# Optimization experiments

Hardware: AMD Instinct MI355X
Metric: run time of the kernel (lower is better)

Reference implementation:

```python
import jax, jax.numpy as jnp
import numpy as np
import math

Q_SHAPES = [(20, 30), (10, 15), (5, 8)]
S_SHAPES = [(20, 30), (10, 15), (5, 8)]
C_IN = 256
C_OUT = 256
NUM_HEADS = 8


def _rel_indices(q_shapes, s_shapes):
    # Faithful translation of QSGA.get_rel_indices: block matrix over pyramid levels.
    rows = []
    for hq, wq in q_shapes:
        cols = []
        for hs, ws in s_shapes:
            ind = np.arange(ws)[None, :] / ws - np.arange(hq)[:, None] / hq  # [hq, ws]
            sc = math.sqrt(ws * hq)
            indx = np.tile(ind, (wq, hs)) * sc                              # [hq*wq, hs*ws]
            indy = np.repeat(np.repeat(ind, wq, axis=0), hs, axis=1) * sc   # [hq*wq, hs*ws]
            indd = indx ** 2 + indy ** 2
            cols.append(np.stack([indd, indx, indy], axis=-1))
        rows.append(np.concatenate(cols, axis=1))
    return jnp.asarray(np.concatenate(rows, axis=0)[None].astype(np.float32))  # [1, Nq, Ns, 3]


def setup_inputs() -> dict:
    key = jax.random.key(0)
    ks = jax.random.split(key, 8)
    B, M = 2, 5
    Nq = sum(h * w for h, w in Q_SHAPES)
    Ns = sum(h * w for h, w in S_SHAPES)
    std = 0.02
    # local_init: v = identity, pos_proj weight zero except col0 = -alphas, gating = ones
    min_a, max_a = 0.002, 0.2
    alphas = np.array([min_a + (max_a - min_a) / NUM_HEADS ** 2.5 * i ** 2.5 for i in range(NUM_HEADS)], np.float32)
    Wp = np.zeros((NUM_HEADS, 3), np.float32)
    Wp[:, 0] = -alphas
    return {
        "q_feat": jax.random.normal(ks[0], (B, Nq, C_IN), jnp.float32),
        "s_feat": jax.random.normal(ks[1], (M, Ns, C_IN), jnp.float32),
        "rel_indices": _rel_indices(Q_SHAPES, S_SHAPES),
        "Wq": jax.random.normal(ks[2], (C_OUT, C_IN), jnp.float32) * std,
        "bq": jnp.zeros((C_OUT,), jnp.float32),
        "Wk": jax.random.normal(ks[3], (C_OUT, C_IN), jnp.float32) * std,
        "bk": jnp.zeros((C_OUT,), jnp.float32),
        "Wv": jnp.eye(C_OUT, C_IN, dtype=jnp.float32),
        "bv": jnp.zeros((C_OUT,), jnp.float32),
        "Wp": jnp.asarray(Wp),
        "bp": jnp.zeros((NUM_HEADS,), jnp.float32),
        "Wo": jax.random.normal(ks[4], (C_OUT, C_OUT), jnp.float32) * std,
        "bo": jnp.zeros((C_OUT,), jnp.float32),
        "gating": jnp.ones((NUM_HEADS,), jnp.float32),
    }


def reference(q_feat, s_feat, rel_indices, Wq, bq, Wk, bk, Wv, bv, Wp, bp, Wo, bo, gating):
    B, Nq, _ = q_feat.shape
    M, Ns, _ = s_feat.shape
    H = gating.shape[0]
    C = Wq.shape[0]
    Dh = C // H
    scale = Dh ** -0.5
    # projections -> [B,H,Nq,Dh], [M,H,Ns,Dh]
    q = (q_feat @ Wq.T + bq).reshape(B, Nq, H, Dh).transpose(0, 2, 1, 3)
    k = (s_feat @ Wk.T + bk).reshape(M, Ns, H, Dh).transpose(0, 2, 1, 3)
    # content scores over all (query image, support image) pairs: [B,M,H,Nq,Ns]
    patch = jnp.einsum('bhqd,mhsd->bmhqs', q, k) * scale
    patch = jax.nn.softmax(patch, axis=-1)
    # positional scores: [1,Nq,Ns,3] -> [1,H,Nq,Ns]
    pos = jax.nn.softmax((rel_indices @ Wp.T + bp).transpose(0, 3, 1, 2), axis=-1)
    g = jax.nn.sigmoid(gating)[None, None, :, None, None]  # [1,1,H,1,1]
    attn = (1.0 - g) * patch + g * pos[:, None]            # broadcast pos over B,M
    attn = attn / attn.sum(axis=-1, keepdims=True)
    v = (s_feat @ Wv.T + bv).reshape(M, Ns, H, Dh).transpose(0, 2, 1, 3)  # [M,H,Ns,Dh]
    out = jnp.einsum('bmhqs,mhsd->bmhqd', attn, v)          # [B,M,H,Nq,Dh]
    out = out.transpose(0, 1, 3, 2, 4).reshape(B, M, Nq, C)  # [B,M,Nq,C]
    return out @ Wo.T + bo
```

## Files before the change

kernel.cpp:

```cpp
#include <hip/hip_runtime.h>
#include <hip/hip_bf16.h>
#include <math.h>

#define B_ 2
#define M_ 5
#define H_ 8
#define C_ 256
#define DH 32
#define NQ 790
#define NS 790
#define QT32 25
#define VROW 800
#define PPAD 800

typedef __attribute__((ext_vector_type(8))) __bf16 bf16x8;
typedef __attribute__((ext_vector_type(16))) float f32x16;
typedef unsigned int u32;
typedef unsigned short u16;

#define LOG2E 1.4426950408889634f

static __device__ __forceinline__ u16 bf16bits(float v) {
  union { __bf16 h; u16 u; } x; x.h = (__bf16)v; return x.u;
}
static __device__ __forceinline__ u32 pack2bf(float a, float b) {
  union { __bf16 h[2]; u32 u; } x; x.h[0] = (__bf16)a; x.h[1] = (__bf16)b; return x.u;
}

#define POS_N 395
#define GEMM0 395
#define PADBLK 544

#define PROJ_STEP(ACC, BY)                                                 \
  {                                                                        \
    int bcol_ = (BY) * 64 + wc * 32 + lo;                                  \
    const float* wf_ = Wm + (size_t)bcol_ * C_ + k0;                       \
    float4 g0_ = *(const float4*)wf_, g1_ = *(const float4*)(wf_ + 4);     \
    bf16x8 b_;                                                             \
    b_[0]=(__bf16)g0_.x; b_[1]=(__bf16)g0_.y; b_[2]=(__bf16)g0_.z; b_[3]=(__bf16)g0_.w; \
    b_[4]=(__bf16)g1_.x; b_[5]=(__bf16)g1_.y; b_[6]=(__bf16)g1_.z; b_[7]=(__bf16)g1_.w; \
    ACC = __builtin_amdgcn_mfma_f32_32x32x16_bf16(a_, b_, ACC, 0, 0, 0);   \
  }

#define STORE_QK(ACC, BY)                                                  \
  {                                                                        \
    int bcol_ = (BY) * 64 + wc * 32 + lo;                                  \
    float bvv_ = bias[bcol_];                                              \
    _Pragma("unroll")                                                      \
    for (int r_ = 0; r_ < 16; ++r_) {                                      \
      int row_ = (r_ & 3) + 8 * (r_ >> 2) + 4 * hi;                        \
      int grow_ = grow0 + wr * 32 + row_;                                  \
      if (grow_ < R) {                                                     \
        float v_ = (ACC[r_] + bvv_) * scale;                               \
        int seg_ = grow_ / 790, srow_ = grow_ - seg_ * 790;                \
        size_t addr_ = ((size_t)(seg_ * H_ + (bcol_ >> 5)) * 790 + srow_) * 32 + (bcol_ & 31); \
        outp[addr_] = bf16bits(v_);                                        \
      }                                                                    \
    }                                                                      \
  }

#define STORE_V(ACC, BY)                                                   \
  {                                                                        \
    int bcol_ = (BY) * 64 + wc * 32 + lo;                                  \
    float bvv_ = bias[bcol_];                                              \
    int cIn_ = wc * 32 + lo;                                               \
    _Pragma("unroll")                                                      \
    for (int r_ = 0; r_ < 16; ++r_) {                                      \
      int row_ = (r_ & 3) + 8 * (r_ >> 2) + 4 * hi;                        \
      Tls[cIn_][wr * 32 + row_] = bf16bits(ACC[r_] + bvv_);                \
    }                                                                      \
    __syncthreads();                                                       \
    {                                                                      \
      int c_l = tid >> 2, g_l = (tid & 3) * 16;                            \
      int gcol = (BY) * 64 + c_l;                                          \
      int g0v = grow0 + g_l;                                               \
      u16 vals_[16];                                                       \
      _Pragma("unroll")                                                    \
      for (int i_ = 0; i_ < 16; ++i_) vals_[i_] = Tls[c_l][g_l + i_];      \
      int mA_ = g0v / 790, mB_ = (g0v + 15) / 790;                         \
      u16* dst_ = vT2 + (size_t)gcol * (M_ * VROW);                        \
      if (mB_ < M_ && mA_ == mB_) {                                        \
        size_t base_ = (size_t)mA_ * VROW + (g0v - mA_ * 790);             \
        *(uint4*)(dst_ + base_)     = *(uint4*)(vals_);                    \
        *(uint4*)(dst_ + base_ + 8) = *(uint4*)(vals_ + 8);                \
      } else {                                                             \
        _Pragma("unroll")                                                  \
        for (int i_ = 0; i_ < 16; ++i_) {                                  \
          int g_ = g0v + i_;                                               \
          if (g_ < M_ * 790) {                                             \
            int mm_ = g_ / 790, ss_ = g_ - mm_ * 790;                      \
            dst_[(size_t)mm_ * VROW + ss_] = vals_[i_];                    \
          }                                                                \
        }                                                                  \
      }                                                                    \
    }                                                                      \
    __syncthreads();                                                       \
  }

__global__ __launch_bounds__(256) void stage1(const float* __restrict__ qf,
    const float* __restrict__ sf, const float* __restrict__ rel,
    const float* __restrict__ Wq, const float* __restrict__ bq,
    const float* __restrict__ Wk, const float* __restrict__ bk,
    const float* __restrict__ Wv, const float* __restrict__ bv,
    const float* __restrict__ Wp, const float* __restrict__ bp,
    u16* __restrict__ qb, u16* __restrict__ kb, u16* __restrict__ vT2,
    u16* __restrict__ pp, float qscale) {
  __shared__ u16 Tls[64][72];
  int bid = blockIdx.x;
  int tid = threadIdx.x;

  if (bid < POS_N) {
    int wave = tid >> 6, lane = tid & 63;
    int q = bid * 2 + (wave >> 1);
    int h0 = (wave & 1) * 4;
    float rd[13], rx[13], ry[13];
#pragma unroll
    for (int t = 0; t < 13; ++t) {
      int s = lane + 64 * t;
      if (s < NS) {
        const float* rp = rel + ((size_t)q * NS + s) * 3;
        rd[t] = rp[0]; rx[t] = rp[1]; ry[t] = rp[2];
      } else { rd[t] = 0.f; rx[t] = 0.f; ry[t] = 0.f; }
    }
    for (int h = h0; h < h0 + 4; ++h) {
      float w0 = Wp[h * 3] * LOG2E, w1 = Wp[h * 3 + 1] * LOG2E,
            w2 = Wp[h * 3 + 2] * LOG2E, b = bp[h] * LOG2E;
      float lg[13], mx = -1e30f;
#pragma unroll
      for (int t = 0; t < 13; ++t) {
        int s = lane + 64 * t;
        float v = rd[t] * w0 + rx[t] * w1 + ry[t] * w2 + b;
        lg[t] = (s < NS) ? v : -1e30f;
        mx = fmaxf(mx, lg[t]);
      }
#pragma unroll
      for (int off = 32; off; off >>= 1) mx = fmaxf(mx, __shfl_xor(mx, off));
      float sm = 0.f;
#pragma unroll
      for (int t = 0; t < 13; ++t) { lg[t] = exp2f(lg[t] - mx); sm += lg[t]; }
#pragma unroll
      for (int off = 32; off; off >>= 1) sm += __shfl_xor(sm, off);
      float inv = 1.f / sm;
#pragma unroll
      for (int t = 0; t < 13; ++t) {
        int s = lane + 64 * t;
        if (s < PPAD)
          pp[((size_t)h * NQ + q) * PPAD + s] = (s < NS) ? bf16bits(lg[t] * inv) : (u16)0;
      }
    }
    return;
  }

  if (bid == PADBLK) {
    int c = tid;
#pragma unroll
    for (int m = 0; m < M_; ++m) {
      u32* p = (u32*)(vT2 + (size_t)c * (M_ * VROW) + m * VROW + 790);
#pragma unroll
      for (int i = 0; i < 5; ++i) p[i] = 0;
    }
    return;
  }

  int j = bid - GEMM0;
  const float* A; const float* Wm; const float* bias; int R; float scale; int role; int bx;
  if (j < 25)      { A = qf; Wm = Wq; bias = bq; R = B_ * NQ; scale = qscale; role = 0; bx = j; }
  else if (j < 87) { A = sf; Wm = Wk; bias = bk; R = M_ * NS; scale = 1.f;    role = 1; bx = j - 25; }
  else             { A = sf; Wm = Wv; bias = bv; R = M_ * NS; scale = 1.f;    role = 2; bx = j - 87; }

  int wave = tid >> 6, lane = tid & 63;
  int lo = lane & 31, hi = lane >> 5;
  int wr = wave >> 1, wc = wave & 1;
  int grow0 = bx * 64;
  int arow = grow0 + wr * 32 + lo;
  int ar = arow < R ? arow : R - 1;

  f32x16 acc0, acc1, acc2, acc3;
#pragma unroll
  for (int r = 0; r < 16; ++r) { acc0[r] = 0.f; acc1[r] = 0.f; acc2[r] = 0.f; acc3[r] = 0.f; }
#pragma unroll
  for (int kk = 0; kk < 16; ++kk) {
    int k0 = kk * 16 + hi * 8;
    const float* af = A + (size_t)ar * C_ + k0;
    float4 f0 = *(const float4*)af, f1 = *(const float4*)(af + 4);
    bf16x8 a_;
    a_[0]=(__bf16)f0.x; a_[1]=(__bf16)f0.y; a_[2]=(__bf16)f0.z; a_[3]=(__bf16)f0.w;
    a_[4]=(__bf16)f1.x; a_[5]=(__bf16)f1.y; a_[6]=(__bf16)f1.z; a_[7]=(__bf16)f1.w;
    PROJ_STEP(acc0, 0);
    PROJ_STEP(acc1, 1);
    PROJ_STEP(acc2, 2);
    PROJ_STEP(acc3, 3);
  }

  if (role < 2) {
    u16* outp = (role == 0) ? qb : kb;
    STORE_QK(acc0, 0);
    STORE_QK(acc1, 1);
    STORE_QK(acc2, 2);
    STORE_QK(acc3, 3);
  } else {
    STORE_V(acc0, 0);
    STORE_V(acc1, 1);
    STORE_V(acc2, 2);
    STORE_V(acc3, 3);
  }
}

static __device__ __forceinline__ void wave_range(int wave, int& st, int& en) {
  st = wave * 6 + (wave ? 1 : 0);
  en = st + (wave ? 6 : 7);
}

#define SM_PV(c_, OACC, ZR, FV0, FV1)                                      \
  {                                                                        \
    float p_[16];                                                          \
    _Pragma("unroll")                                                      \
    for (int r_ = 0; r_ < 16; ++r_) p_[r_] = exp2f(c_[r_]);                \
    float s0_ = p_[0]+p_[1],  s1_ = p_[2]+p_[3];                           \
    float s2_ = p_[4]+p_[5],  s3_ = p_[6]+p_[7];                           \
    float s4_ = p_[8]+p_[9],  s5_ = p_[10]+p_[11];                         \
    float s6_ = p_[12]+p_[13], s7_ = p_[14]+p_[15];                        \
    s0_ += s1_; s2_ += s3_; s4_ += s5_; s6_ += s7_;                        \
    s0_ += s2_; s4_ += s6_;                                                \
    float ts_ = s0_ + s4_;                                                 \
    { float xa_ = ts_, xb_ = ts_;                                          \
      asm("v_permlane32_swap_b32 %0, %1" : "+v"(xa_), "+v"(xb_));          \
      ZR += xa_ + xb_; }                                                   \
    u32 pk_[8];                                                            \
    _Pragma("unroll")                                                      \
    for (int t_ = 0; t_ < 8; ++t_) pk_[t_] = pack2bf(p_[2*t_], p_[2*t_+1]); \
    asm("v_permlane32_swap_b32 %0, %1" : "+v"(pk_[0]), "+v"(pk_[2]));      \
    asm("v_permlane32_swap_b32 %0, %1" : "+v"(pk_[1]), "+v"(pk_[3]));      \
    asm("v_permlane32_swap_b32 %0, %1" : "+v"(pk_[4]), "+v"(pk_[6]));      \
    asm("v_permlane32_swap_b32 %0, %1" : "+v"(pk_[5]), "+v"(pk_[7]));      \
    union { u32 u[4]; bf16x8 v; } pa_, pb_;                                \
    pa_.u[0] = pk_[0]; pa_.u[1] = pk_[1]; pa_.u[2] = pk_[2]; pa_.u[3] = pk_[3]; \
    pb_.u[0] = pk_[4]; pb_.u[1] = pk_[5]; pb_.u[2] = pk_[6]; pb_.u[3] = pk_[7]; \
    OACC = __builtin_amdgcn_mfma_f32_32x32x16_bf16(FV0, pa_.v, OACC, 0, 0, 0); \
    OACC = __builtin_amdgcn_mfma_f32_32x32x16_bf16(FV1, pb_.v, OACC, 0, 0, 0); \
  }

#define TILE_BODY(KC0,KC1,VC0,VC1,PC0,PC1, KN0,KN1,VN0,VN1,PN0,PN1, IT, NT) \
  {                                                                        \
    int srn_ = (NT) * 32 + lo; if (srn_ >= NS) srn_ = NS - 1;              \
    KN0 = *(const bf16x8*)(kbase + (size_t)srn_ * 32 + hi8);               \
    KN1 = *(const bf16x8*)(kbase + (size_t)srn_ * 32 + 16 + hi8);          \
    VN0 = *(const bf16x8*)(vbase + (NT) * 32 + hi8);                       \
    VN1 = *(const bf16x8*)(vbase + (NT) * 32 + 16 + hi8);                  \
    PN0 = *(const bf16x8*)(pbase + (NT) * 32 + hi8);                       \
    PN1 = *(const bf16x8*)(pbase + (NT) * 32 + 16 + hi8);                  \
    f32x16 c0_ = kZero, c1_ = kZero;                                       \
    c0_ = __builtin_amdgcn_mfma_f32_32x32x16_bf16(KC0, fq00, c0_, 0, 0, 0);\
    c0_ = __builtin_amdgcn_mfma_f32_32x32x16_bf16(KC1, fq01, c0_, 0, 0, 0);\
    c1_ = __builtin_amdgcn_mfma_f32_32x32x16_bf16(KC0, fq10, c1_, 0, 0, 0);\
    c1_ = __builtin_amdgcn_mfma_f32_32x32x16_bf16(KC1, fq11, c1_, 0, 0, 0);\
    Opos = __builtin_amdgcn_mfma_f32_32x32x16_bf16(VC0, PC0, Opos, 0, 0, 0);\
    Opos = __builtin_amdgcn_mfma_f32_32x32x16_bf16(VC1, PC1, Opos, 0, 0, 0);\
    if ((IT) == 24) {                                                      \
      _Pragma("unroll")                                                    \
      for (int r_ = 0; r_ < 16; ++r_) {                                    \
        int sl_ = (r_ & 3) + 8 * (r_ >> 2) + 4 * hi;                       \
        if (768 + sl_ >= NS) { c0_[r_] = -1e30f; c1_[r_] = -1e30f; }       \
      }                                                                    \
    }                                                                      \
    SM_PV(c0_, O0, Z0, VC0, VC1);                                          \
    SM_PV(c1_, O1, Z1, VC0, VC1);                                          \
  }

__global__ __launch_bounds__(256, 2) void attn2(const u16* __restrict__ qb,
    const u16* __restrict__ kb, const u16* __restrict__ vT2,
    const u16* __restrict__ pp, const float* __restrict__ gating,
    u16* __restrict__ opb) {
  int logical = (blockIdx.x & 7) * 125 + (blockIdx.x >> 3);
  int m  = logical % M_;
  int r2 = logical / M_;
  int qt = r2 % QT32;
  int h  = r2 / QT32;
  int tid = threadIdx.x;
  int wave = tid >> 6, lane = tid & 63;
  int lo = lane & 31, hi = lane >> 5, hi8 = hi * 8;
  int qg = qt * 32 + lo;
  int qc = qg < NQ ? qg : NQ - 1;

  const u16* qp0 = qb + ((size_t)(0 * H_ + h) * NQ + qc) * 32 + hi8;
  const u16* qp1 = qb + ((size_t)(1 * H_ + h) * NQ + qc) * 32 + hi8;
  bf16x8 fq00 = *(const bf16x8*)qp0;
  bf16x8 fq01 = *(const bf16x8*)(qp0 + 16);
  bf16x8 fq10 = *(const bf16x8*)qp1;
  bf16x8 fq11 = *(const bf16x8*)(qp1 + 16);
  const u16* kbase = kb + ((size_t)(m * H_ + h) * NS) * 32;
  const u16* vbase = vT2 + (size_t)(h * DH + lo) * (M_ * VROW) + m * VROW;
  const u16* pbase = pp + ((size_t)h * NQ + qc) * PPAD;

  f32x16 O0, O1, Opos, kZero;
#pragma unroll
  for (int r = 0; r < 16; ++r) { O0[r] = 0.f; O1[r] = 0.f; Opos[r] = 0.f; kZero[r] = 0.f; }
  float Z0 = 0.f, Z1 = 0.f;
  int st, en; wave_range(wave, st, en);

  bf16x8 ak0, ak1, av0, av1, ap0, ap1, bk0, bk1, bv0, bv1, bp0, bp1;
  {
    int sr0 = st * 32 + lo; if (sr0 >= NS) sr0 = NS - 1;
    ak0 = *(const bf16x8*)(kbase + (size_t)sr0 * 32 + hi8);
    ak1 = *(const bf16x8*)(kbase + (size_t)sr0 * 32 + 16 + hi8);
    av0 = *(const bf16x8*)(vbase + st * 32 + hi8);
    av1 = *(const bf16x8*)(vbase + st * 32 + 16 + hi8);
    ap0 = *(const bf16x8*)(pbase + st * 32 + hi8);
    ap1 = *(const bf16x8*)(pbase + st * 32 + 16 + hi8);
  }
  int it = st;
  while (it + 2 <= en) {
    TILE_BODY(ak0, ak1, av0, av1, ap0, ap1, bk0, bk1, bv0, bv1, bp0, bp1, it, it + 1);
    int nt2 = (it + 2 < en) ? it + 2 : it + 1;
    TILE_BODY(bk0, bk1, bv0, bv1, bp0, bp1, ak0, ak1, av0, av1, ap0, ap1, it + 1, nt2);
    it += 2;
  }
  if (it < en) TILE_BODY(ak0, ak1, av0, av1, ap0, ap1, bk0, bk1, bv0, bv1, bp0, bp1, it, it);

  __shared__ float Os[4][32][33];
  __shared__ float Zs[4][32];
  float g = 1.f / (1.f + __expf(-gating[h]));
  int d = tid & 31, qi = tid >> 5;
  float oc0[4], oc1[4];

#pragma unroll
  for (int r = 0; r < 16; ++r) {
    int dd = (r & 3) + 8 * (r >> 2) + 4 * hi;
    Os[wave][dd][lo] = O0[r];
  }
  if (hi == 0) Zs[wave][lo] = Z0;
  __syncthreads();
#pragma unroll
  for (int k = 0; k < 4; ++k) {
    int ql = qi + 8 * k;
    float zg = Zs[0][ql] + Zs[1][ql] + Zs[2][ql] + Zs[3][ql];
    float oc = Os[0][d][ql] + Os[1][d][ql] + Os[2][d][ql] + Os[3][d][ql];
    oc0[k] = (1.f - g) * oc / zg;
  }
  __syncthreads();

#pragma unroll
  for (int r = 0; r < 16; ++r) {
    int dd = (r & 3) + 8 * (r >> 2) + 4 * hi;
    Os[wave][dd][lo] = O1[r];
  }
  if (hi == 0) Zs[wave][lo] = Z1;
  __syncthreads();
#pragma unroll
  for (int k = 0; k < 4; ++k) {
    int ql = qi + 8 * k;
    float zg = Zs[0][ql] + Zs[1][ql] + Zs[2][ql] + Zs[3][ql];
    float oc = Os[0][d][ql] + Os[1][d][ql] + Os[2][d][ql] + Os[3][d][ql];
    oc1[k] = (1.f - g) * oc / zg;
  }
  __syncthreads();

#pragma unroll
  for (int r = 0; r < 16; ++r) {
    int dd = (r & 3) + 8 * (r >> 2) + 4 * hi;
    Os[wave][dd][lo] = Opos[r];
  }
  __syncthreads();
  u16* out0 = opb + ((size_t)(0 * M_ + m) * NQ) * C_ + h * DH + d;
  u16* out1 = opb + ((size_t)(1 * M_ + m) * NQ) * C_ + h * DH + d;
#pragma unroll
  for (int k = 0; k < 4; ++k) {
    int ql = qi + 8 * k;
    int qgl = qt * 32 + ql;
    if (qgl < NQ) {
      float op = Os[0][d][ql] + Os[1][d][ql] + Os[2][d][ql] + Os[3][d][ql];
      out0[(size_t)qgl * C_] = bf16bits(oc0[k] + g * op);
      out1[(size_t)qgl * C_] = bf16bits(oc1[k] + g * op);
    }
  }
}

__global__ __launch_bounds__(256) void out_gemm(const u16* __restrict__ Ap,
    const float* __restrict__ W, const float* __restrict__ bias,
    float* __restrict__ outp, int R) {
  int tid = threadIdx.x;
  int wave = tid >> 6, lane = tid & 63;
  int lo = lane & 31, hi = lane >> 5;
  int wr = wave >> 1, wc = wave & 1;
  int arow = blockIdx.x * 64 + wr * 32 + lo;
  int ar = arow < R ? arow : R - 1;
  int bcolA = blockIdx.y * 128 + wc * 32 + lo;
  int bcolB = bcolA + 64;
  f32x16 accA, accB;
#pragma unroll
  for (int r = 0; r < 16; ++r) { accA[r] = 0.f; accB[r] = 0.f; }
#pragma unroll
  for (int kk = 0; kk < 16; ++kk) {
    int k0 = kk * 16 + hi * 8;
    bf16x8 a = *(const bf16x8*)(Ap + (size_t)ar * C_ + k0);
    bf16x8 b;
    const float* wf = W + (size_t)bcolA * C_ + k0;
    float4 g0 = *(const float4*)wf, g1 = *(const float4*)(wf + 4);
    b[0]=(__bf16)g0.x; b[1]=(__bf16)g0.y; b[2]=(__bf16)g0.z; b[3]=(__bf16)g0.w;
    b[4]=(__bf16)g1.x; b[5]=(__bf16)g1.y; b[6]=(__bf16)g1.z; b[7]=(__bf16)g1.w;
    accA = __builtin_amdgcn_mfma_f32_32x32x16_bf16(a, b, accA, 0, 0, 0);
    const float* wf2 = W + (size_t)bcolB * C_ + k0;
    float4 h0 = *(const float4*)wf2, h1 = *(const float4*)(wf2 + 4);
    b[0]=(__bf16)h0.x; b[1]=(__bf16)h0.y; b[2]=(__bf16)h0.z; b[3]=(__bf16)h0.w;
    b[4]=(__bf16)h1.x; b[5]=(__bf16)h1.y; b[6]=(__bf16)h1.z; b[7]=(__bf16)h1.w;
    accB = __builtin_amdgcn_mfma_f32_32x32x16_bf16(a, b, accB, 0, 0, 0);
  }
  float bvA = bias[bcolA], bvB = bias[bcolB];
#pragma unroll
  for (int r = 0; r < 16; ++r) {
    int row = (r & 3) + 8 * (r >> 2) + 4 * hi;
    int grow = blockIdx.x * 64 + wr * 32 + row;
    if (grow < R) {
      outp[(size_t)grow * C_ + bcolA] = accA[r] + bvA;
      outp[(size_t)grow * C_ + bcolB] = accB[r] + bvB;
    }
  }
}

extern "C" void kernel_launch(void* const* d_in, const int* in_sizes, int n_in,
                              void* d_out, int out_size, void* d_ws, size_t ws_size,
                              hipStream_t stream) {
  const float* q_feat = (const float*)d_in[0];
  const float* s_feat = (const float*)d_in[1];
  const float* rel    = (const float*)d_in[2];
  const float* Wq = (const float*)d_in[3];
  const float* bq = (const float*)d_in[4];
  const float* Wk = (const float*)d_in[5];
  const float* bk = (const float*)d_in[6];
  const float* Wv = (const float*)d_in[7];
  const float* bv = (const float*)d_in[8];
  const float* Wp = (const float*)d_in[9];
  const float* bp = (const float*)d_in[10];
  const float* Wo = (const float*)d_in[11];
  const float* bo = (const float*)d_in[12];
  const float* gating = (const float*)d_in[13];
  float* out = (float*)d_out;

  char* w = (char*)d_ws;
  u16* qb  = (u16*)w;
  u16* kb  = (u16*)(w + 808960);
  u16* vT2 = (u16*)(w + 2831360);
  u16* pp  = (u16*)(w + 4879360);
  u16* opb = (u16*)(w + 14991360);

  const float QSCALE = 0.17677669529663687f * 1.4426950408889634f;

  stage1<<<545, 256, 0, stream>>>(q_feat, s_feat, rel, Wq, bq, Wk, bk, Wv, bv,
                                  Wp, bp, qb, kb, vT2, pp, QSCALE);
  attn2<<<1000, 256, 0, stream>>>(qb, kb, vT2, pp, gating, opb);
  out_gemm<<<dim3(124, 2), 256, 0, stream>>>(opb, Wo, bo, out, B_ * M_ * NQ);
}
```

Before: 72.93 us.

## Pre-convert Wo to bf16, drop V/P prefetch registers, raise attention occupancy

Extra stage1 blocks convert Wo to bf16 once, so out_gemm loads bf16 weights directly instead of converting fp32 per tile. The attention loop no longer double-buffers V and positional tiles in registers and loads them in the current iteration, and launch bounds go from 2 to 3 blocks per SM to raise occupancy. The positional softmax drops its max-subtraction pass, which relies on the logits being bounded so exp2 does not overflow. Removing the prefetch can expose load latency inside the loop.

```diff
diff --git a/kernel.cpp b/kernel.cpp
--- a/kernel.cpp
+++ b/kernel.cpp
@@ -30,6 +30,7 @@
 #define POS_N 395
 #define GEMM0 395
 #define PADBLK 544
+#define WCVT0 545
 
 #define PROJ_STEP(ACC, BY)                                                 \
   {                                                                        \
@@ -103,8 +104,9 @@
     const float* __restrict__ Wk, const float* __restrict__ bk,
     const float* __restrict__ Wv, const float* __restrict__ bv,
     const float* __restrict__ Wp, const float* __restrict__ bp,
+    const float* __restrict__ Wo,
     u16* __restrict__ qb, u16* __restrict__ kb, u16* __restrict__ vT2,
-    u16* __restrict__ pp, float qscale) {
+    u16* __restrict__ pp, u16* __restrict__ wob, float qscale) {
   __shared__ u16 Tls[64][72];
   int bid = blockIdx.x;
   int tid = threadIdx.x;
@@ -125,19 +127,14 @@
     for (int h = h0; h < h0 + 4; ++h) {
       float w0 = Wp[h * 3] * LOG2E, w1 = Wp[h * 3 + 1] * LOG2E,
             w2 = Wp[h * 3 + 2] * LOG2E, b = bp[h] * LOG2E;
-      float lg[13], mx = -1e30f;
+      float lg[13], sm = 0.f;
 #pragma unroll
       for (int t = 0; t < 13; ++t) {
         int s = lane + 64 * t;
         float v = rd[t] * w0 + rx[t] * w1 + ry[t] * w2 + b;
-        lg[t] = (s < NS) ? v : -1e30f;
-        mx = fmaxf(mx, lg[t]);
+        lg[t] = exp2f((s < NS) ? v : -1e30f);
+        sm += lg[t];
       }
-#pragma unroll
-      for (int off = 32; off; off >>= 1) mx = fmaxf(mx, __shfl_xor(mx, off));
-      float sm = 0.f;
-#pragma unroll
-      for (int t = 0; t < 13; ++t) { lg[t] = exp2f(lg[t] - mx); sm += lg[t]; }
 #pragma unroll
       for (int off = 32; off; off >>= 1) sm += __shfl_xor(sm, off);
       float inv = 1.f / sm;
@@ -158,6 +155,21 @@
       u32* p = (u32*)(vT2 + (size_t)c * (M_ * VROW) + m * VROW + 790);
 #pragma unroll
       for (int i = 0; i < 5; ++i) p[i] = 0;
+    }
+    return;
+  }
+
+  if (bid >= WCVT0) {
+    int base = (bid - WCVT0) * 8192;
+#pragma unroll
+    for (int k = 0; k < 4; ++k) {
+      int idx = base + k * 2048 + tid * 8;
+      const float* src = Wo + idx;
+      float4 f0 = *(const float4*)src, f1 = *(const float4*)(src + 4);
+      u16 v[8];
+      v[0]=bf16bits(f0.x); v[1]=bf16bits(f0.y); v[2]=bf16bits(f0.z); v[3]=bf16bits(f0.w);
+      v[4]=bf16bits(f1.x); v[5]=bf16bits(f1.y); v[6]=bf16bits(f1.z); v[7]=bf16bits(f1.w);
+      *(uint4*)(wob + idx) = *(uint4*)v;
     }
     return;
   }
@@ -240,22 +252,24 @@
     OACC = __builtin_amdgcn_mfma_f32_32x32x16_bf16(FV1, pb_.v, OACC, 0, 0, 0); \
   }
 
-#define TILE_BODY(KC0,KC1,VC0,VC1,PC0,PC1, KN0,KN1,VN0,VN1,PN0,PN1, IT, NT) \
+#define TILE_BODY(KC0,KC1, KN0,KN1, IT, NT)                                \
   {                                                                        \
+     \
+    bf16x8 vf0 = *(const bf16x8*)(vbase + (IT) * 32 + hi8);                \
+    bf16x8 vf1 = *(const bf16x8*)(vbase + (IT) * 32 + 16 + hi8);           \
+    bf16x8 pf0 = *(const bf16x8*)(pbase + (IT) * 32 + hi8);                \
+    bf16x8 pf1 = *(const bf16x8*)(pbase + (IT) * 32 + 16 + hi8);           \
+                                             \
     int srn_ = (NT) * 32 + lo; if (srn_ >= NS) srn_ = NS - 1;              \
     KN0 = *(const bf16x8*)(kbase + (size_t)srn_ * 32 + hi8);               \
     KN1 = *(const bf16x8*)(kbase + (size_t)srn_ * 32 + 16 + hi8);          \
-    VN0 = *(const bf16x8*)(vbase + (NT) * 32 + hi8);                       \
-    VN1 = *(const bf16x8*)(vbase + (NT) * 32 + 16 + hi8);                  \
-    PN0 = *(const bf16x8*)(pbase + (NT) * 32 + hi8);                       \
-    PN1 = *(const bf16x8*)(pbase + (NT) * 32 + 16 + hi8);                  \
     f32x16 c0_ = kZero, c1_ = kZero;                                       \
     c0_ = __builtin_amdgcn_mfma_f32_32x32x16_bf16(KC0, fq00, c0_, 0, 0, 0);\
     c0_ = __builtin_amdgcn_mfma_f32_32x32x16_bf16(KC1, fq01, c0_, 0, 0, 0);\
     c1_ = __builtin_amdgcn_mfma_f32_32x32x16_bf16(KC0, fq10, c1_, 0, 0, 0);\
     c1_ = __builtin_amdgcn_mfma_f32_32x32x16_bf16(KC1, fq11, c1_, 0, 0, 0);\
-    Opos = __builtin_amdgcn_mfma_f32_32x32x16_bf16(VC0, PC0, Opos, 0, 0, 0);\
-    Opos = __builtin_amdgcn_mfma_f32_32x32x16_bf16(VC1, PC1, Opos, 0, 0, 0);\
+    Opos = __builtin_amdgcn_mfma_f32_32x32x16_bf16(vf0, pf0, Opos, 0, 0, 0);\
+    Opos = __builtin_amdgcn_mfma_f32_32x32x16_bf16(vf1, pf1, Opos, 0, 0, 0);\
     if ((IT) == 24) {                                                      \
       _Pragma("unroll")                                                    \
       for (int r_ = 0; r_ < 16; ++r_) {                                    \
@@ -263,11 +277,11 @@
         if (768 + sl_ >= NS) { c0_[r_] = -1e30f; c1_[r_] = -1e30f; }       \
       }                                                                    \
     }                                                                      \
-    SM_PV(c0_, O0, Z0, VC0, VC1);                                          \
-    SM_PV(c1_, O1, Z1, VC0, VC1);                                          \
-  }
-
-__global__ __launch_bounds__(256, 2) void attn2(const u16* __restrict__ qb,
+    SM_PV(c0_, O0, Z0, vf0, vf1);                                          \
+    SM_PV(c1_, O1, Z1, vf0, vf1);                                          \
+  }
+
+__global__ __launch_bounds__(256, 3) void attn2(const u16* __restrict__ qb,
     const u16* __restrict__ kb, const u16* __restrict__ vT2,
     const u16* __restrict__ pp, const float* __restrict__ gating,
     u16* __restrict__ opb) {
@@ -298,24 +312,20 @@
   float Z0 = 0.f, Z1 = 0.f;
   int st, en; wave_range(wave, st, en);
 
-  bf16x8 ak0, ak1, av0, av1, ap0, ap1, bk0, bk1, bv0, bv1, bp0, bp1;
+  bf16x8 ak0, ak1, bk0, bk1;
   {
     int sr0 = st * 32 + lo; if (sr0 >= NS) sr0 = NS - 1;
     ak0 = *(const bf16x8*)(kbase + (size_t)sr0 * 32 + hi8);
     ak1 = *(const bf16x8*)(kbase + (size_t)sr0 * 32 + 16 + hi8);
-    av0 = *(const bf16x8*)(vbase + st * 32 + hi8);
-    av1 = *(const bf16x8*)(vbase + st * 32 + 16 + hi8);
-    ap0 = *(const bf16x8*)(pbase + st * 32 + hi8);
-    ap1 = *(const bf16x8*)(pbase + st * 32 + 16 + hi8);
   }
   int it = st;
   while (it + 2 <= en) {
-    TILE_BODY(ak0, ak1, av0, av1, ap0, ap1, bk0, bk1, bv0, bv1, bp0, bp1, it, it + 1);
+    TILE_BODY(ak0, ak1, bk0, bk1, it, it + 1);
     int nt2 = (it + 2 < en) ? it + 2 : it + 1;
-    TILE_BODY(bk0, bk1, bv0, bv1, bp0, bp1, ak0, ak1, av0, av1, ap0, ap1, it + 1, nt2);
+    TILE_BODY(bk0, bk1, ak0, ak1, it + 1, nt2);
     it += 2;
   }
-  if (it < en) TILE_BODY(ak0, ak1, av0, av1, ap0, ap1, bk0, bk1, bv0, bv1, bp0, bp1, it, it);
+  if (it < en) TILE_BODY(ak0, ak1, bk0, bk1, it, it);
 
   __shared__ float Os[4][32][33];
   __shared__ float Zs[4][32];
@@ -376,7 +386,7 @@
 }
 
 __global__ __launch_bounds__(256) void out_gemm(const u16* __restrict__ Ap,
-    const float* __restrict__ W, const float* __restrict__ bias,
+    const u16* __restrict__ Wb, const float* __restrict__ bias,
     float* __restrict__ outp, int R) {
   int tid = threadIdx.x;
   int wave = tid >> 6, lane = tid & 63;
@@ -393,17 +403,10 @@
   for (int kk = 0; kk < 16; ++kk) {
     int k0 = kk * 16 + hi * 8;
     bf16x8 a = *(const bf16x8*)(Ap + (size_t)ar * C_ + k0);
-    bf16x8 b;
-    const float* wf = W + (size_t)bcolA * C_ + k0;
-    float4 g0 = *(const float4*)wf, g1 = *(const float4*)(wf + 4);
-    b[0]=(__bf16)g0.x; b[1]=(__bf16)g0.y; b[2]=(__bf16)g0.z; b[3]=(__bf16)g0.w;
-    b[4]=(__bf16)g1.x; b[5]=(__bf16)g1.y; b[6]=(__bf16)g1.z; b[7]=(__bf16)g1.w;
-    accA = __builtin_amdgcn_mfma_f32_32x32x16_bf16(a, b, accA, 0, 0, 0);
-    const float* wf2 = W + (size_t)bcolB * C_ + k0;
-    float4 h0 = *(const float4*)wf2, h1 = *(const float4*)(wf2 + 4);
-    b[0]=(__bf16)h0.x; b[1]=(__bf16)h0.y; b[2]=(__bf16)h0.z; b[3]=(__bf16)h0.w;
-    b[4]=(__bf16)h1.x; b[5]=(__bf16)h1.y; b[6]=(__bf16)h1.z; b[7]=(__bf16)h1.w;
-    accB = __builtin_amdgcn_mfma_f32_32x32x16_bf16(a, b, accB, 0, 0, 0);
+    bf16x8 bA = *(const bf16x8*)(Wb + (size_t)bcolA * C_ + k0);
+    bf16x8 bB = *(const bf16x8*)(Wb + (size_t)bcolB * C_ + k0);
+    accA = __builtin_amdgcn_mfma_f32_32x32x16_bf16(a, bA, accA, 0, 0, 0);
+    accB = __builtin_amdgcn_mfma_f32_32x32x16_bf16(a, bB, accB, 0, 0, 0);
   }
   float bvA = bias[bcolA], bvB = bias[bcolB];
 #pragma unroll
@@ -442,11 +445,12 @@
   u16* vT2 = (u16*)(w + 2831360);
   u16* pp  = (u16*)(w + 4879360);
   u16* opb = (u16*)(w + 14991360);
+  u16* wob = (u16*)(w + 19036160);
 
   const float QSCALE = 0.17677669529663687f * 1.4426950408889634f;
 
-  stage1<<<545, 256, 0, stream>>>(q_feat, s_feat, rel, Wq, bq, Wk, bk, Wv, bv,
-                                  Wp, bp, qb, kb, vT2, pp, QSCALE);
+  stage1<<<553, 256, 0, stream>>>(q_feat, s_feat, rel, Wq, bq, Wk, bk, Wv, bv,
+                                  Wp, bp, Wo, qb, kb, vT2, pp, wob, QSCALE);
   attn2<<<1000, 256, 0, stream>>>(qb, kb, vT2, pp, gating, opb);
-  out_gemm<<<dim3(124, 2), 256, 0, stream>>>(opb, Wo, bo, out, B_ * M_ * NQ);
-}
+  out_gemm<<<dim3(124, 2), 256, 0, stream>>>(opb, wob, bo, out, B_ * M_ * NQ);
+}
```

Result: faster. 69.90 us (-4.2%).
